# Performance work log

Measured on AMD Instinct MI355X. Metric: run time of the kernel, lower is better.

The kernel has to match this reference:

```python
import jax, jax.numpy as jnp
import numpy as np

NUM_ELEMENTS = 100
EMBED_DIM = 256
HIDDEN_DIM = 512
NUM_HEADS = 8
NUM_MASKS = 1
NUM_GAUSSIANS = 50
RBF_RADIUS = 12.0
N_ATOMS = 50000
N_PAIRS = 500000


def setup_inputs() -> dict:
    key = jax.random.key(0)
    ks = jax.random.split(key, 10)
    anum = jax.random.randint(ks[0], (N_ATOMS,), 0, NUM_ELEMENTS)
    row_index = jax.random.randint(ks[1], (N_PAIRS,), 0, N_ATOMS)
    col_index = jax.random.randint(ks[2], (N_PAIRS,), 0, N_ATOMS)
    dist = jax.random.uniform(ks[3], (N_PAIRS,), jnp.float32) * RBF_RADIUS
    s = 0.02
    W_rbf = jax.random.normal(ks[4], (NUM_GAUSSIANS, HIDDEN_DIM), jnp.float32) * s
    b_rbf = jnp.zeros((HIDDEN_DIM,), jnp.float32)
    emb_table = jax.random.normal(ks[5], (NUM_ELEMENTS * NUM_ELEMENTS, EMBED_DIM), jnp.float32) * s
    W1 = jax.random.normal(ks[6], (HIDDEN_DIM + EMBED_DIM, HIDDEN_DIM), jnp.float32) * s
    b1 = jnp.zeros((HIDDEN_DIM,), jnp.float32)
    W2 = jax.random.normal(ks[7], (HIDDEN_DIM, NUM_HEADS * NUM_MASKS), jnp.float32) * s
    b2 = jnp.zeros((NUM_HEADS * NUM_MASKS,), jnp.float32)
    return dict(anum=anum, row_index=row_index, col_index=col_index, dist=dist,
                W_rbf=W_rbf, b_rbf=b_rbf, emb_table=emb_table,
                W1=W1, b1=b1, W2=W2, b2=b2)


def reference(anum, row_index, col_index, dist, W_rbf, b_rbf, emb_table, W1, b1, W2, b2):
    # --- RadialBasisFunction: Gaussian smearing + linear projection to hidden_dim ---
    offsets = jnp.linspace(0.0, RBF_RADIUS, NUM_GAUSSIANS, dtype=dist.dtype)  # [G]
    coeff = -0.5 / (offsets[1] - offsets[0]) ** 2
    g = jnp.exp(coeff * (dist[:, None] - offsets) ** 2)          # [E, G]
    rbf = g @ W_rbf + b_rbf                                      # [E, H]
    # --- pair-type embedding gather ---
    pair_id = anum[row_index] + NUM_ELEMENTS * anum[col_index]   # [E]
    emb = emb_table[pair_id]                                     # [E, D]
    # --- gated residual MLP: fc1 -> silu -> gate by rbf -> fc2 ---
    x = jnp.concatenate([rbf, emb], axis=1)                      # [E, H+D]
    h = jax.nn.silu(x @ W1 + b1) * rbf                           # [E, H]
    att_bias = h @ W2 + b2                                       # [E, heads*masks]
    att_bias = att_bias.reshape(dist.shape[0], NUM_HEADS, NUM_MASKS)
    return jnp.transpose(att_bias, (2, 1, 0))                    # [masks, heads, E]
```

## Files before the change

kernel.cpp:

```cpp
#include <hip/hip_runtime.h>
#include <hip/hip_bf16.h>

#define NGAUSS   50
#define HID      512
#define EMBD     256
#define NPID     10000
#define EBLK     64
#define GPAD     72
#define EPAD     264

typedef __attribute__((ext_vector_type(8))) short   bfrag;
typedef __attribute__((ext_vector_type(4))) float   facc;
typedef __attribute__((ext_vector_type(8))) unsigned short u16x8;
typedef __attribute__((ext_vector_type(4))) unsigned short u16x4;

#define PBF_OFF    0
#define WC32_OFF   10240000
#define W1BF_OFF   10344448
#define WRBF_OFF   10606592
#define WCBF_OFF   10672128
#define W2F_OFF    10737664

static __device__ __forceinline__ unsigned short f2bf(float f) {
    union { float f; unsigned u; } v; v.f = f;
    unsigned r = v.u + 0x7FFF + ((v.u >> 16) & 1);
    return (unsigned short)(r >> 16);
}
static __device__ __forceinline__ unsigned pack2bf(float a, float b) {
    __hip_bfloat162 t = __float22bfloat162_rn(make_float2(a, b));
    return *reinterpret_cast<unsigned*>(&t);
}
static __device__ __forceinline__ float bfu_lo(unsigned u) {
    union { unsigned u; float f; } v; v.u = u << 16; return v.f;
}
static __device__ __forceinline__ float bfu_hi(unsigned u) {
    union { unsigned u; float f; } v; v.u = u & 0xFFFF0000u; return v.f;
}

__global__ __launch_bounds__(256) void prep0(
    const float* __restrict__ W_rbf, const float* __restrict__ b_rbf,
    const float* __restrict__ W1, const float* __restrict__ b1,
    const float* __restrict__ W2, char* __restrict__ ws)
{
    const int b = blockIdx.x, tid = threadIdx.x;
    if (b < 102) {
        const int j = b >> 1, chalf = b & 1;
        const int c = chalf * 256 + tid;
        const float* row = (j < NGAUSS) ? &W_rbf[(size_t)j * HID] : b_rbf;
        float a0 = 0.f, a1 = 0.f, a2 = 0.f, a3 = 0.f;
        for (int k = 0; k < HID; k += 4) {
            a0 += row[k + 0] * W1[(size_t)(k + 0) * HID + c];
            a1 += row[k + 1] * W1[(size_t)(k + 1) * HID + c];
            a2 += row[k + 2] * W1[(size_t)(k + 2) * HID + c];
            a3 += row[k + 3] * W1[(size_t)(k + 3) * HID + c];
        }
        float acc = (a0 + a1) + (a2 + a3);
        ((float*)(ws + WC32_OFF))[j * HID + c] = (j < NGAUSS) ? acc : acc + b1[c];
    } else if (b < 166) {
        const int gid = (b - 102) * 256 + tid;
        const int lane = gid & 63, tmp = gid >> 6, nt = tmp & 31, kt = tmp >> 5;
        const int c  = nt * 16 + (lane & 15);
        const int kb = HID + kt * 32 + ((lane >> 4) << 3);
        unsigned short* dst = (unsigned short*)(ws + W1BF_OFF);
        #pragma unroll
        for (int j = 0; j < 8; ++j)
            dst[(size_t)gid * 8 + j] = f2bf(W1[(size_t)(kb + j) * HID + c]);
    } else if (b < 182) {
        const int gid = (b - 166) * 256 + tid;
        const int lane = gid & 63, tmp = gid >> 6, nt = tmp & 31, kt = tmp >> 5;
        const int c  = nt * 16 + (lane & 15);
        const int kb = kt * 32 + ((lane >> 4) << 3);
        unsigned short* dst = (unsigned short*)(ws + WRBF_OFF);
        #pragma unroll
        for (int j = 0; j < 8; ++j) {
            int k = kb + j;
            unsigned short v = 0;
            if (k < NGAUSS)       v = f2bf(W_rbf[(size_t)k * HID + c]);
            else if (k == NGAUSS) v = f2bf(b_rbf[c]);
            dst[(size_t)gid * 8 + j] = v;
        }
    } else {
        const int gid = (b - 182) * 256 + tid;
        const int lane = gid & 63, kt = gid >> 6;
        const int col = lane & 15;
        const int kb  = kt * 32 + ((lane >> 4) << 3);
        unsigned short* dst = (unsigned short*)(ws + W2F_OFF);
        #pragma unroll
        for (int j = 0; j < 8; ++j)
            dst[(size_t)gid * 8 + j] = (col < 8) ? f2bf(W2[(size_t)(kb + j) * 8 + col]) : (unsigned short)0;
    }
}

__global__ __launch_bounds__(512) void prep1(
    const float* __restrict__ emb_table, char* __restrict__ ws)
{
    const int b = blockIdx.x, t = threadIdx.x;
    if (b < 8) {
        const int gid = b * 512 + t;
        const int lane = gid & 63, tmp = gid >> 6, nt = tmp & 31, kt = tmp >> 5;
        const int c  = nt * 16 + (lane & 15);
        const int kb = kt * 32 + ((lane >> 4) << 3);
        const float* wc = (const float*)(ws + WC32_OFF);
        unsigned short* dst = (unsigned short*)(ws + WCBF_OFF);
        #pragma unroll
        for (int j = 0; j < 8; ++j) {
            int k = kb + j;
            dst[(size_t)gid * 8 + j] = (k <= NGAUSS) ? f2bf(wc[k * HID + c]) : (unsigned short)0;
        }
        return;
    }
    __shared__ unsigned short s_e[64 * EPAD];
    const int pb = b - 8;
    const int lane = t & 63, w = t >> 6;
    const int lq = lane >> 4, lr = lane & 15;
    {
        int row = t >> 3;
        int grow = pb * 64 + row; if (grow >= NPID) grow = NPID - 1;
        int c0 = (t & 7) * 32;
        #pragma unroll
        for (int ii = 0; ii < 8; ++ii) {
            const float4 v = *(const float4*)&emb_table[(size_t)grow * EMBD + c0 + ii * 4];
            u16x4 bv; bv[0] = f2bf(v.x); bv[1] = f2bf(v.y); bv[2] = f2bf(v.z); bv[3] = f2bf(v.w);
            *(u16x4*)&s_e[row * EPAD + c0 + ii * 4] = bv;
        }
    }
    __syncthreads();
    const int ntb = w * 4;
    const unsigned short* W1bf = (const unsigned short*)(ws + W1BF_OFF);
    unsigned short* Pbf = (unsigned short*)(ws + PBF_OFF);
    facc acc[4][4] = {};
    for (int kt = 0; kt < 8; ++kt) {
        bfrag a[4];
        #pragma unroll
        for (int mt = 0; mt < 4; ++mt)
            a[mt] = *(const bfrag*)&s_e[(mt * 16 + lr) * EPAD + kt * 32 + lq * 8];
        #pragma unroll
        for (int ntl = 0; ntl < 4; ++ntl) {
            bfrag bv = *(const bfrag*)&W1bf[((size_t)(kt * 32 + ntb + ntl) * 64 + lane) * 8];
            #pragma unroll
            for (int mt = 0; mt < 4; ++mt)
                acc[mt][ntl] = __builtin_amdgcn_mfma_f32_16x16x32_bf16(a[mt], bv, acc[mt][ntl], 0, 0, 0);
        }
    }
    #pragma unroll
    for (int ntl = 0; ntl < 4; ++ntl) {
        const int col = (ntb + ntl) * 16 + lr;
        const int Wd = col >> 6, Md = (col >> 4) & 3, Ld = (col >> 2) & 3, Jd = col & 3;
        const int off = Wd * 64 + Ld * 16 + Md * 4 + Jd;
        #pragma unroll
        for (int mt = 0; mt < 4; ++mt) {
            #pragma unroll
            for (int r = 0; r < 4; ++r) {
                int grow = pb * 64 + mt * 16 + lq * 4 + r;
                if (grow < NPID) Pbf[(size_t)grow * HID + off] = f2bf(acc[mt][ntl][r]);
            }
        }
    }
}

__global__ __launch_bounds__(512, 4) void pair_embed_mfma(
    const int* __restrict__ anum,
    const int* __restrict__ row_index,
    const int* __restrict__ col_index,
    const float* __restrict__ dist,
    const float* __restrict__ b2,
    const char* __restrict__ ws,
    float* __restrict__ out,
    int n)
{
    extern __shared__ char smem[];
    unsigned short* s_buf = (unsigned short*)smem;
    unsigned short* s_g   = (unsigned short*)(smem + 65536);
    float*          s_scr = (float*)(smem + 65536 + 64 * GPAD * 2);
    float*          s_d   = (float*)(smem + 65536 + 64 * GPAD * 2 + 4096);
    int*            s_pid = (int*)(smem + 65536 + 64 * GPAD * 2 + 4096 + 256);

    const unsigned short* Pbf   = (const unsigned short*)(ws + PBF_OFF);
    const unsigned short* Wrbff = (const unsigned short*)(ws + WRBF_OFF);
    const unsigned short* Wcbf  = (const unsigned short*)(ws + WCBF_OFF);
    const unsigned short* W2f   = (const unsigned short*)(ws + W2F_OFF);

    const int t = threadIdx.x, lane = t & 63, w = t >> 6;
    const int e0 = blockIdx.x * EBLK;
    const int lq = lane >> 4, lr = lane & 15;

    if (t < EBLK) {
        int e = e0 + t; if (e >= n) e = n - 1;
        s_d[t] = dist[e];
        s_pid[t] = anum[row_index[e]] + 100 * anum[col_index[e]];
    }
    __syncthreads();

    const size_t pbase_off = (size_t)(w * 64 + lq * 16);
    uint4 q0, q1;
    {
        const unsigned short* prow = Pbf + (size_t)s_pid[lr] * HID + pbase_off;
        q0 = *(const uint4*)&prow[0];
        q1 = *(const uint4*)&prow[8];
    }

    {
        const float sp = 12.0f / 49.0f;
        const float coeff = -0.5f / (sp * sp);
        int e = t >> 3, j0 = (t & 7) * 8;
        float d = s_d[e];
        float gv[8];
        #pragma unroll
        for (int j = 0; j < 8; ++j) {
            int jj = j0 + j;
            float v = d - (float)jj * sp;
            gv[j] = (jj < NGAUSS) ? __expf(coeff * v * v) : (jj == NGAUSS ? 1.0f : 0.0f);
        }
        uint4 pk;
        pk.x = pack2bf(gv[0], gv[1]); pk.y = pack2bf(gv[2], gv[3]);
        pk.z = pack2bf(gv[4], gv[5]); pk.w = pack2bf(gv[6], gv[7]);
        *(uint4*)&s_g[e * GPAD + j0] = pk;
    }

    const int mtb = w * 4;
    bfrag aR[2][4], aC[2][4];
    #pragma unroll
    for (int kt = 0; kt < 2; ++kt)
        #pragma unroll
        for (int m = 0; m < 4; ++m) {
            aR[kt][m] = *(const bfrag*)&Wrbff[((size_t)(kt * 32 + mtb + m) * 64 + lane) * 8];
            aC[kt][m] = *(const bfrag*)&Wcbf [((size_t)(kt * 32 + mtb + m) * 64 + lane) * 8];
        }
    __syncthreads();

    const int hbase = w * 1024 + (lq >> 1) * 128 + lr * 8 + (lq & 1) * 4;

    for (int nt4 = 0; nt4 < 4; ++nt4) {
        const uint4 c0 = q0, c1 = q1;
        if (nt4 < 3) {
            const unsigned short* prow = Pbf + (size_t)s_pid[(nt4 + 1) * 16 + lr] * HID + pbase_off;
            q0 = *(const uint4*)&prow[0];
            q1 = *(const uint4*)&prow[8];
        }
        const int e = nt4 * 16 + lr;
        bfrag g0 = *(const bfrag*)&s_g[e * GPAD + lq * 8];
        bfrag g1 = *(const bfrag*)&s_g[e * GPAD + 32 + lq * 8];
        facc racc[4] = {}, cacc[4] = {};
        #pragma unroll
        for (int m = 0; m < 4; ++m) {
            racc[m] = __builtin_amdgcn_mfma_f32_16x16x32_bf16(aR[0][m], g0, racc[m], 0, 0, 0);
            cacc[m] = __builtin_amdgcn_mfma_f32_16x16x32_bf16(aC[0][m], g0, cacc[m], 0, 0, 0);
        }
        #pragma unroll
        for (int m = 0; m < 4; ++m) {
            racc[m] = __builtin_amdgcn_mfma_f32_16x16x32_bf16(aR[1][m], g1, racc[m], 0, 0, 0);
            cacc[m] = __builtin_amdgcn_mfma_f32_16x16x32_bf16(aC[1][m], g1, cacc[m], 0, 0, 0);
        }
        const uint2 pv[4] = { make_uint2(c0.x, c0.y), make_uint2(c0.z, c0.w),
                              make_uint2(c1.x, c1.y), make_uint2(c1.z, c1.w) };
        unsigned short* hb = s_buf + nt4 * 8192 + hbase;
        #pragma unroll
        for (int m = 0; m < 4; ++m) {
            float p0 = bfu_lo(pv[m].x), p1 = bfu_hi(pv[m].x);
            float p2 = bfu_lo(pv[m].y), p3 = bfu_hi(pv[m].y);
            float pr0 = cacc[m][0] + p0, pr1 = cacc[m][1] + p1;
            float pr2 = cacc[m][2] + p2, pr3 = cacc[m][3] + p3;
            float h0 = pr0 * __builtin_amdgcn_rcpf(1.0f + __expf(-pr0)) * racc[m][0];
            float h1 = pr1 * __builtin_amdgcn_rcpf(1.0f + __expf(-pr1)) * racc[m][1];
            float h2 = pr2 * __builtin_amdgcn_rcpf(1.0f + __expf(-pr2)) * racc[m][2];
            float h3 = pr3 * __builtin_amdgcn_rcpf(1.0f + __expf(-pr3)) * racc[m][3];
            uint2 hw;
            hw.x = pack2bf(h0, h1);
            hw.y = pack2bf(h2, h3);
            *(uint2*)&hb[m * 256] = hw;
        }
    }
    __syncthreads();

    {
        const int nt4 = w & 3;
        const int ks  = w >> 2;
        const unsigned short* hbuf = s_buf + nt4 * 8192;
        facc a4 = {};
        #pragma unroll
        for (int kq = 0; kq < 8; ++kq) {
            int kt = ks * 8 + kq;
            bfrag hfrag = *(const bfrag*)&hbuf[(kt * 64 + lane) * 8];
            bfrag wfrag = *(const bfrag*)&W2f[((size_t)kt * 64 + lane) * 8];
            a4 = __builtin_amdgcn_mfma_f32_16x16x32_bf16(wfrag, hfrag, a4, 0, 0, 0);
        }
        if (ks == 1) *(facc*)&s_scr[(nt4 * 64 + lane) * 4] = a4;
        __syncthreads();
        if (ks == 0 && lq < 2) {
            facc oth = *(const facc*)&s_scr[(nt4 * 64 + lane) * 4];
            const int e = e0 + nt4 * 16 + lr;
            if (e < n) {
                #pragma unroll
                for (int r = 0; r < 4; ++r) {
                    int head = lq * 4 + r;
                    out[(size_t)head * n + e] = a4[r] + oth[r] + b2[head];
                }
            }
        }
    }
}

extern "C" void kernel_launch(void* const* d_in, const int* in_sizes, int n_in,
                              void* d_out, int out_size, void* d_ws, size_t ws_size,
                              hipStream_t stream) {
    const int*   anum      = (const int*)d_in[0];
    const int*   row_index = (const int*)d_in[1];
    const int*   col_index = (const int*)d_in[2];
    const float* dist      = (const float*)d_in[3];
    const float* W_rbf     = (const float*)d_in[4];
    const float* b_rbf     = (const float*)d_in[5];
    const float* emb_table = (const float*)d_in[6];
    const float* W1        = (const float*)d_in[7];
    const float* b1        = (const float*)d_in[8];
    const float* W2        = (const float*)d_in[9];
    const float* b2        = (const float*)d_in[10];
    float* out = (float*)d_out;
    char* ws = (char*)d_ws;

    const int n_edges = in_sizes[3];

    prep0<<<186, 256, 0, stream>>>(W_rbf, b_rbf, W1, b1, W2, ws);
    prep1<<<8 + 157, 512, 0, stream>>>(emb_table, ws);

    const int grid = (n_edges + EBLK - 1) / EBLK;
    const size_t lds_bytes = 65536 + 64 * GPAD * 2 + 4096 + 256 + 256;
    pair_embed_mfma<<<grid, 512, lds_bytes, stream>>>(
        anum, row_index, col_index, dist, b2, ws, out, n_edges);
}
```

Measured before the change: 185.8 us.

## Double block to 1024 threads, halve per-wave tiles, four-way fc2 K-split

Doubles the threads per block so each wave handles 2 instead of 4 hidden m-tiles in the RBF/fc1 stage. Each wave now loads one 16-byte projection chunk per edge tile, and the fc2 reduction is split four ways over K with partial sums reduced through shared memory. The scratch buffer is aliased onto the Gaussian buffer, which is no longer needed by then, so LDS per block stays about the same while waves per CU roughly double. This raises occupancy and latency hiding. In exchange it adds an extra LDS reduction step and a tighter register budget from the launch bounds. SiLU is also rewritten in vector form using exp2f.

```diff
diff --git a/kernel.cpp b/kernel.cpp
--- a/kernel.cpp
+++ b/kernel.cpp
@@ -1,5 +1,6 @@
 #include <hip/hip_runtime.h>
 #include <hip/hip_bf16.h>
+#include <math.h>
 
 #define NGAUSS   50
 #define HID      512
@@ -158,7 +159,7 @@
     }
 }
 
-__global__ __launch_bounds__(512, 4) void pair_embed_mfma(
+__global__ __launch_bounds__(1024, 8) void pair_embed_mfma(
     const int* __restrict__ anum,
     const int* __restrict__ row_index,
     const int* __restrict__ col_index,
@@ -171,9 +172,9 @@
     extern __shared__ char smem[];
     unsigned short* s_buf = (unsigned short*)smem;
     unsigned short* s_g   = (unsigned short*)(smem + 65536);
-    float*          s_scr = (float*)(smem + 65536 + 64 * GPAD * 2);
-    float*          s_d   = (float*)(smem + 65536 + 64 * GPAD * 2 + 4096);
-    int*            s_pid = (int*)(smem + 65536 + 64 * GPAD * 2 + 4096 + 256);
+    float*          s_scr = (float*)(smem + 65536);
+    float*          s_d   = (float*)(smem + 65536 + 12288);
+    int*            s_pid = (int*)(smem + 65536 + 12288 + 256);
 
     const unsigned short* Pbf   = (const unsigned short*)(ws + PBF_OFF);
     const unsigned short* Wrbff = (const unsigned short*)(ws + WRBF_OFF);
@@ -191,84 +192,90 @@
     }
     __syncthreads();
 
-    const size_t pbase_off = (size_t)(w * 64 + lq * 16);
-    uint4 q0, q1;
-    {
-        const unsigned short* prow = Pbf + (size_t)s_pid[lr] * HID + pbase_off;
-        q0 = *(const uint4*)&prow[0];
-        q1 = *(const uint4*)&prow[8];
-    }
+    const int pbase = (w >> 1) * 64 + lq * 16 + (w & 1) * 8;
+    uint4 q = *(const uint4*)&Pbf[(unsigned)s_pid[lr] * 512u + pbase];
 
     {
         const float sp = 12.0f / 49.0f;
         const float coeff = -0.5f / (sp * sp);
-        int e = t >> 3, j0 = (t & 7) * 8;
+        int e = t >> 4, j0 = (t & 15) * 4;
         float d = s_d[e];
-        float gv[8];
-        #pragma unroll
-        for (int j = 0; j < 8; ++j) {
+        float gv[4];
+        #pragma unroll
+        for (int j = 0; j < 4; ++j) {
             int jj = j0 + j;
             float v = d - (float)jj * sp;
             gv[j] = (jj < NGAUSS) ? __expf(coeff * v * v) : (jj == NGAUSS ? 1.0f : 0.0f);
         }
-        uint4 pk;
+        uint2 pk;
         pk.x = pack2bf(gv[0], gv[1]); pk.y = pack2bf(gv[2], gv[3]);
-        pk.z = pack2bf(gv[4], gv[5]); pk.w = pack2bf(gv[6], gv[7]);
-        *(uint4*)&s_g[e * GPAD + j0] = pk;
-    }
-
-    const int mtb = w * 4;
-    bfrag aR[2][4], aC[2][4];
+        *(uint2*)&s_g[e * GPAD + j0] = pk;
+    }
+
+    const int mtb = w * 2;
+    bfrag aR[2][2], aC[2][2];
     #pragma unroll
     for (int kt = 0; kt < 2; ++kt)
         #pragma unroll
-        for (int m = 0; m < 4; ++m) {
+        for (int m = 0; m < 2; ++m) {
             aR[kt][m] = *(const bfrag*)&Wrbff[((size_t)(kt * 32 + mtb + m) * 64 + lane) * 8];
             aC[kt][m] = *(const bfrag*)&Wcbf [((size_t)(kt * 32 + mtb + m) * 64 + lane) * 8];
         }
     __syncthreads();
 
-    const int hbase = w * 1024 + (lq >> 1) * 128 + lr * 8 + (lq & 1) * 4;
+    const int hbase = w * 512 + (lq >> 1) * 128 + lr * 8 + (lq & 1) * 4;
 
     for (int nt4 = 0; nt4 < 4; ++nt4) {
-        const uint4 c0 = q0, c1 = q1;
-        if (nt4 < 3) {
-            const unsigned short* prow = Pbf + (size_t)s_pid[(nt4 + 1) * 16 + lr] * HID + pbase_off;
-            q0 = *(const uint4*)&prow[0];
-            q1 = *(const uint4*)&prow[8];
-        }
+        uint4 qn;
+        if (nt4 < 3)
+            qn = *(const uint4*)&Pbf[(unsigned)s_pid[(nt4 + 1) * 16 + lr] * 512u + pbase];
         const int e = nt4 * 16 + lr;
         bfrag g0 = *(const bfrag*)&s_g[e * GPAD + lq * 8];
         bfrag g1 = *(const bfrag*)&s_g[e * GPAD + 32 + lq * 8];
-        facc racc[4] = {}, cacc[4] = {};
-        #pragma unroll
-        for (int m = 0; m < 4; ++m) {
+        facc racc[2] = {}, cacc[2] = {};
+        #pragma unroll
+        for (int m = 0; m < 2; ++m) {
             racc[m] = __builtin_amdgcn_mfma_f32_16x16x32_bf16(aR[0][m], g0, racc[m], 0, 0, 0);
             cacc[m] = __builtin_amdgcn_mfma_f32_16x16x32_bf16(aC[0][m], g0, cacc[m], 0, 0, 0);
         }
         #pragma unroll
-        for (int m = 0; m < 4; ++m) {
+        for (int m = 0; m < 2; ++m) {
             racc[m] = __builtin_amdgcn_mfma_f32_16x16x32_bf16(aR[1][m], g1, racc[m], 0, 0, 0);
             cacc[m] = __builtin_amdgcn_mfma_f32_16x16x32_bf16(aC[1][m], g1, cacc[m], 0, 0, 0);
         }
-        const uint2 pv[4] = { make_uint2(c0.x, c0.y), make_uint2(c0.z, c0.w),
-                              make_uint2(c1.x, c1.y), make_uint2(c1.z, c1.w) };
+        facc pf0, pf1;
+        pf0[0] = bfu_lo(q.x); pf0[1] = bfu_hi(q.x); pf0[2] = bfu_lo(q.y); pf0[3] = bfu_hi(q.y);
+        pf1[0] = bfu_lo(q.z); pf1[1] = bfu_hi(q.z); pf1[2] = bfu_lo(q.w); pf1[3] = bfu_hi(q.w);
         unsigned short* hb = s_buf + nt4 * 8192 + hbase;
-        #pragma unroll
-        for (int m = 0; m < 4; ++m) {
-            float p0 = bfu_lo(pv[m].x), p1 = bfu_hi(pv[m].x);
-            float p2 = bfu_lo(pv[m].y), p3 = bfu_hi(pv[m].y);
-            float pr0 = cacc[m][0] + p0, pr1 = cacc[m][1] + p1;
-            float pr2 = cacc[m][2] + p2, pr3 = cacc[m][3] + p3;
-            float h0 = pr0 * __builtin_amdgcn_rcpf(1.0f + __expf(-pr0)) * racc[m][0];
-            float h1 = pr1 * __builtin_amdgcn_rcpf(1.0f + __expf(-pr1)) * racc[m][1];
-            float h2 = pr2 * __builtin_amdgcn_rcpf(1.0f + __expf(-pr2)) * racc[m][2];
-            float h3 = pr3 * __builtin_amdgcn_rcpf(1.0f + __expf(-pr3)) * racc[m][3];
-            uint2 hw;
-            hw.x = pack2bf(h0, h1);
-            hw.y = pack2bf(h2, h3);
-            *(uint2*)&hb[m * 256] = hw;
-        }
+        {
+            facc pre = cacc[0] + pf0;
+            facc nx  = pre * -1.442695040888963f;
+            facc ex;
+            #pragma unroll
+            for (int i = 0; i < 4; ++i) ex[i] = exp2f(nx[i]);
+            facc den = ex + 1.0f;
+            facc sg;
+            #pragma unroll
+            for (int i = 0; i < 4; ++i) sg[i] = __builtin_amdgcn_rcpf(den[i]);
+            facc h = pre * sg * racc[0];
+            uint2 hw; hw.x = pack2bf(h[0], h[1]); hw.y = pack2bf(h[2], h[3]);
+            *(uint2*)&hb[0] = hw;
+        }
+        {
+            facc pre = cacc[1] + pf1;
+            facc nx  = pre * -1.442695040888963f;
+            facc ex;
+            #pragma unroll
+            for (int i = 0; i < 4; ++i) ex[i] = exp2f(nx[i]);
+            facc den = ex + 1.0f;
+            facc sg;
+            #pragma unroll
+            for (int i = 0; i < 4; ++i) sg[i] = __builtin_amdgcn_rcpf(den[i]);
+            facc h = pre * sg * racc[1];
+            uint2 hw; hw.x = pack2bf(h[0], h[1]); hw.y = pack2bf(h[2], h[3]);
+            *(uint2*)&hb[256] = hw;
+        }
+        if (nt4 < 3) q = qn;
     }
     __syncthreads();
 
@@ -278,22 +285,28 @@
         const unsigned short* hbuf = s_buf + nt4 * 8192;
         facc a4 = {};
         #pragma unroll
-        for (int kq = 0; kq < 8; ++kq) {
-            int kt = ks * 8 + kq;
+        for (int kq = 0; kq < 4; ++kq) {
+            int kt = ks * 4 + kq;
             bfrag hfrag = *(const bfrag*)&hbuf[(kt * 64 + lane) * 8];
             bfrag wfrag = *(const bfrag*)&W2f[((size_t)kt * 64 + lane) * 8];
             a4 = __builtin_amdgcn_mfma_f32_16x16x32_bf16(wfrag, hfrag, a4, 0, 0, 0);
         }
-        if (ks == 1) *(facc*)&s_scr[(nt4 * 64 + lane) * 4] = a4;
+        if (ks > 0) *(facc*)&s_scr[(((ks - 1) * 4 + nt4) * 64 + lane) * 4] = a4;
         __syncthreads();
-        if (ks == 0 && lq < 2) {
-            facc oth = *(const facc*)&s_scr[(nt4 * 64 + lane) * 4];
-            const int e = e0 + nt4 * 16 + lr;
-            if (e < n) {
-                #pragma unroll
-                for (int r = 0; r < 4; ++r) {
-                    int head = lq * 4 + r;
-                    out[(size_t)head * n + e] = a4[r] + oth[r] + b2[head];
+        if (ks == 0) {
+            #pragma unroll
+            for (int p = 0; p < 3; ++p) {
+                facc oth = *(const facc*)&s_scr[((size_t)(p * 4 + nt4) * 64 + lane) * 4];
+                a4 += oth;
+            }
+            if (lq < 2) {
+                const int e = e0 + nt4 * 16 + lr;
+                if (e < n) {
+                    #pragma unroll
+                    for (int r = 0; r < 4; ++r) {
+                        int head = lq * 4 + r;
+                        out[(size_t)head * n + e] = a4[r] + b2[head];
+                    }
                 }
             }
         }
@@ -323,7 +336,7 @@
     prep1<<<8 + 157, 512, 0, stream>>>(emb_table, ws);
 
     const int grid = (n_edges + EBLK - 1) / EBLK;
-    const size_t lds_bytes = 65536 + 64 * GPAD * 2 + 4096 + 256 + 256;
-    pair_embed_mfma<<<grid, 512, lds_bytes, stream>>>(
+    const size_t lds_bytes = 65536 + 12288 + 256 + 256;
+    pair_embed_mfma<<<grid, 1024, lds_bytes, stream>>>(
         anum, row_index, col_index, dist, b2, ws, out, n_edges);
 }
```

After: 519.3 us. +179.5%, slower.
